# Performance work log

Hardware: AMD Instinct MI355X
Metric: run time of the kernel (lower is better)

## Reference

```python
import jax, jax.numpy as jnp
import numpy as np

K_SPARSE = 64  # number of units kept active per row

def setup_inputs() -> dict:
    key = jax.random.key(0)
    x = jax.random.normal(key, (16384, 4096), dtype=jnp.float32)
    return {"x": x}

def reference(x) -> jnp.ndarray:
    # Training-phase path of KSparse.call -> k_sparsify:
    # kth_smallest = sort(x)[..., n-1-k]  (the (k+1)-th largest value per row)
    # out = x * (x > kth_smallest)
    n = x.shape[-1]
    sorted_x = jnp.sort(x, axis=-1)              # ascending, [B, D]
    kth = sorted_x[:, n - 1 - K_SPARSE]          # [B]
    mask = (x > kth[:, None]).astype(x.dtype)    # strictly greater, as in source
    return x * mask
```

## Files before the change

### kernel.cpp

```cpp
#include <hip/hip_runtime.h>

#define K_SPARSE 64
#define COLS     4096
#define NTHREADS 256
#define EPT      (COLS / NTHREADS)
#define VPT      (EPT / 4)
#define FAST_CAP 1024
#define LIST_CAP (FAST_CAP + 8)

typedef float    nfloat4 __attribute__((ext_vector_type(4)));

__device__ __forceinline__ unsigned mapf(unsigned b) {
    return (b & 0x80000000u) ? ~b : (b | 0x80000000u);
}

__global__ __launch_bounds__(NTHREADS)
void ksparse_select(const float* __restrict__ x, float* __restrict__ out, int rows)
{
    const int row = blockIdx.x;
    if (row >= rows) return;
    const int t    = threadIdx.x;
    const int lane = t & 63;
    const int w    = t >> 6;

    __shared__ __align__(16) float list[LIST_CAP];
    __shared__ unsigned wtot[4];
    __shared__ float s_kth;

    const float4* __restrict__ xrow =
        reinterpret_cast<const float4*>(x) + (size_t)row * (COLS / 4);
    nfloat4* __restrict__ orow =
        reinterpret_cast<nfloat4*>(out) + (size_t)row * (COLS / 4);

    float f[EPT];
#pragma unroll
    for (int i = 0; i < VPT; ++i) {
        float4 v = xrow[t + i * NTHREADS];
        f[i * 4 + 0] = v.x; f[i * 4 + 1] = v.y;
        f[i * 4 + 2] = v.z; f[i * 4 + 3] = v.w;
    }

    __builtin_amdgcn_s_setprio(1);

    float fT = 0.0f; unsigned cnt = 0, base = 0, c = 0;
#pragma unroll
    for (int r = 0; r < 2; ++r) {
        fT = (r == 0) ? 1.9f : 0.9f;
        cnt = 0;
#pragma unroll
        for (int i = 0; i < EPT; ++i) cnt += (f[i] > fT) ? 1u : 0u;

        unsigned s = cnt;
#pragma unroll
        for (int off = 1; off < 64; off <<= 1) {
            unsigned v = __shfl_up(s, off, 64);
            if (lane >= off) s += v;
        }
        if (lane == 63) wtot[w] = s;
        __syncthreads();
        const unsigned c0 = wtot[0], c1 = wtot[1], c2 = wtot[2], c3 = wtot[3];
        c = c0 + c1 + c2 + c3;
        if (c >= K_SPARSE + 1 || r == 1) {
            base = (w > 0 ? c0 : 0u) + (w > 1 ? c1 : 0u) + (w > 2 ? c2 : 0u)
                 + s - cnt;
            break;
        }
        __syncthreads();
    }

    float kth;
    if (c >= K_SPARSE + 1 && c <= FAST_CAP) {
        unsigned pos = base;
#pragma unroll
        for (int i = 0; i < EPT; ++i) {
            if (f[i] > fT) list[pos++] = f[i];
        }
        if (t < 8) list[c + t] = -1.0e38f;
        __syncthreads();

        const int nq = (int)((c + 3) >> 2);
        const nfloat4* listv = reinterpret_cast<const nfloat4*>(list);
        for (int j = t; j < (int)c; j += NTHREADS) {
            const float vj = list[j];
            unsigned g = 0, e = 0;
            for (int q = 0; q < nq; ++q) {
                const nfloat4 ql = listv[q];
                g += (ql.x > vj) + (ql.y > vj) + (ql.z > vj) + (ql.w > vj);
                e += (ql.x == vj) + (ql.y == vj) + (ql.z == vj) + (ql.w == vj);
            }
            if (g <= (unsigned)K_SPARSE && (unsigned)K_SPARSE < g + e)
                s_kth = vj;
        }
        __syncthreads();
        kth = s_kth;
    } else {
        unsigned prefix = 0u;
        for (int b = 31; b >= 0; --b) {
            const unsigned trial = prefix | (1u << b);
            unsigned c2 = 0;
#pragma unroll
            for (int i = 0; i < EPT; ++i)
                c2 += (mapf(__float_as_uint(f[i])) >= trial) ? 1u : 0u;
#pragma unroll
            for (int off = 32; off >= 1; off >>= 1)
                c2 += __shfl_xor(c2, off, 64);
            if (lane == 0) wtot[w] = c2;
            __syncthreads();
            const unsigned tot = wtot[0] + wtot[1] + wtot[2] + wtot[3];
            if (tot >= K_SPARSE + 1) prefix = trial;
            __syncthreads();
        }
        const unsigned kb = (prefix & 0x80000000u) ? (prefix ^ 0x80000000u) : ~prefix;
        kth = __uint_as_float(kb);
    }

    __builtin_amdgcn_s_setprio(0);

#pragma unroll
    for (int i = 0; i < VPT; ++i) {
        nfloat4 o;
        o.x = (f[i * 4 + 0] > kth) ? f[i * 4 + 0] : 0.0f;
        o.y = (f[i * 4 + 1] > kth) ? f[i * 4 + 1] : 0.0f;
        o.z = (f[i * 4 + 2] > kth) ? f[i * 4 + 2] : 0.0f;
        o.w = (f[i * 4 + 3] > kth) ? f[i * 4 + 3] : 0.0f;
        __builtin_nontemporal_store(o, &orow[t + i * NTHREADS]);
    }
}

extern "C" void kernel_launch(void* const* d_in, const int* in_sizes, int n_in,
                              void* d_out, int out_size, void* d_ws, size_t ws_size,
                              hipStream_t stream) {
    const float* x = (const float*)d_in[0];
    float* out = (float*)d_out;
    const int rows = in_sizes[0] / COLS;
    ksparse_select<<<rows, NTHREADS, 0, stream>>>(x, out, rows);
}
```

Baseline: 72.59 us.

## Store zero vectors early, replace syncthreads with LDS-only barriers, drop setprio

In the common fast path, each thread stores zeros right away for any float4 with no element above the pre-threshold, overlapping those writes with the selection phase, and writes only the remaining float4s after kth is known. __syncthreads is replaced by a barrier that waits only on LDS counters, so outstanding global stores are not drained at every barrier. The s_setprio calls are removed. The early zeros are correct because kth is at least the pre-threshold, but the fast path now has more branching.

Result: slower. 157.5 us (+116.9%).

```diff
diff --git a/kernel.cpp b/kernel.cpp
--- a/kernel.cpp
+++ b/kernel.cpp
@@ -8,10 +8,16 @@
 #define FAST_CAP 1024
 #define LIST_CAP (FAST_CAP + 8)
 
-typedef float    nfloat4 __attribute__((ext_vector_type(4)));
+typedef float nfloat4 __attribute__((ext_vector_type(4)));
 
 __device__ __forceinline__ unsigned mapf(unsigned b) {
     return (b & 0x80000000u) ? ~b : (b | 0x80000000u);
+}
+
+__device__ __forceinline__ void lbar() {
+    asm volatile("s_waitcnt lgkmcnt(0)" ::: "memory");
+    __builtin_amdgcn_s_barrier();
+    __builtin_amdgcn_sched_barrier(0);
 }
 
 __global__ __launch_bounds__(NTHREADS)
@@ -40,8 +46,6 @@
         f[i * 4 + 2] = v.z; f[i * 4 + 3] = v.w;
     }
 
-    __builtin_amdgcn_s_setprio(1);
-
     float fT = 0.0f; unsigned cnt = 0, base = 0, c = 0;
 #pragma unroll
     for (int r = 0; r < 2; ++r) {
@@ -57,7 +61,7 @@
             if (lane >= off) s += v;
         }
         if (lane == 63) wtot[w] = s;
-        __syncthreads();
+        lbar();
         const unsigned c0 = wtot[0], c1 = wtot[1], c2 = wtot[2], c3 = wtot[3];
         c = c0 + c1 + c2 + c3;
         if (c >= K_SPARSE + 1 || r == 1) {
@@ -65,18 +69,29 @@
                  + s - cnt;
             break;
         }
-        __syncthreads();
+        lbar();
     }
 
-    float kth;
     if (c >= K_SPARSE + 1 && c <= FAST_CAP) {
+        unsigned hm = 0;
+#pragma unroll
+        for (int i = 0; i < VPT; ++i) {
+            const bool has = (f[i*4+0] > fT) | (f[i*4+1] > fT)
+                           | (f[i*4+2] > fT) | (f[i*4+3] > fT);
+            if (has) hm |= (1u << i);
+            else {
+                nfloat4 z = {0.0f, 0.0f, 0.0f, 0.0f};
+                __builtin_nontemporal_store(z, &orow[t + i * NTHREADS]);
+            }
+        }
+
         unsigned pos = base;
 #pragma unroll
         for (int i = 0; i < EPT; ++i) {
             if (f[i] > fT) list[pos++] = f[i];
         }
         if (t < 8) list[c + t] = -1.0e38f;
-        __syncthreads();
+        lbar();
 
         const int nq = (int)((c + 3) >> 2);
         const nfloat4* listv = reinterpret_cast<const nfloat4*>(list);
@@ -91,8 +106,20 @@
             if (g <= (unsigned)K_SPARSE && (unsigned)K_SPARSE < g + e)
                 s_kth = vj;
         }
-        __syncthreads();
-        kth = s_kth;
+        lbar();
+        const float kth = s_kth;
+
+#pragma unroll
+        for (int i = 0; i < VPT; ++i) {
+            if (hm & (1u << i)) {
+                nfloat4 o;
+                o.x = (f[i*4+0] > kth) ? f[i*4+0] : 0.0f;
+                o.y = (f[i*4+1] > kth) ? f[i*4+1] : 0.0f;
+                o.z = (f[i*4+2] > kth) ? f[i*4+2] : 0.0f;
+                o.w = (f[i*4+3] > kth) ? f[i*4+3] : 0.0f;
+                __builtin_nontemporal_store(o, &orow[t + i * NTHREADS]);
+            }
+        }
     } else {
         unsigned prefix = 0u;
         for (int b = 31; b >= 0; --b) {
@@ -105,25 +132,23 @@
             for (int off = 32; off >= 1; off >>= 1)
                 c2 += __shfl_xor(c2, off, 64);
             if (lane == 0) wtot[w] = c2;
-            __syncthreads();
+            lbar();
             const unsigned tot = wtot[0] + wtot[1] + wtot[2] + wtot[3];
             if (tot >= K_SPARSE + 1) prefix = trial;
-            __syncthreads();
+            lbar();
         }
         const unsigned kb = (prefix & 0x80000000u) ? (prefix ^ 0x80000000u) : ~prefix;
-        kth = __uint_as_float(kb);
-    }
-
-    __builtin_amdgcn_s_setprio(0);
+        const float kth = __uint_as_float(kb);
 
 #pragma unroll
-    for (int i = 0; i < VPT; ++i) {
-        nfloat4 o;
-        o.x = (f[i * 4 + 0] > kth) ? f[i * 4 + 0] : 0.0f;
-        o.y = (f[i * 4 + 1] > kth) ? f[i * 4 + 1] : 0.0f;
-        o.z = (f[i * 4 + 2] > kth) ? f[i * 4 + 2] : 0.0f;
-        o.w = (f[i * 4 + 3] > kth) ? f[i * 4 + 3] : 0.0f;
-        __builtin_nontemporal_store(o, &orow[t + i * NTHREADS]);
+        for (int i = 0; i < VPT; ++i) {
+            nfloat4 o;
+            o.x = (f[i*4+0] > kth) ? f[i*4+0] : 0.0f;
+            o.y = (f[i*4+1] > kth) ? f[i*4+1] : 0.0f;
+            o.z = (f[i*4+2] > kth) ? f[i*4+2] : 0.0f;
+            o.w = (f[i*4+3] > kth) ? f[i*4+3] : 0.0f;
+            __builtin_nontemporal_store(o, &orow[t + i * NTHREADS]);
+        }
     }
 }
 
```
